# Performance work log

Hardware: AMD Instinct MI355X
Metric: run time of the kernel (lower is better)

The kernel has to match this reference:

```python
import jax, jax.numpy as jnp
import numpy as np

B, C, H, W = 64, 64, 64, 64
KD = 64  # kernel_dim == res == dim (required by the torch reshapes)


def _ln(t, g, b, eps=1e-5):
    mu = jnp.mean(t, axis=-1, keepdims=True)
    var = jnp.var(t, axis=-1, keepdims=True)
    return (t - mu) * jax.lax.rsqrt(var + eps) * g + b


def _cos_map(n, kd):
    i = jnp.arange(n, dtype=jnp.float32)[:, None]
    j = jnp.arange(kd, dtype=jnp.float32)[None, :]
    return jnp.cos(i * j * jnp.pi / n) / kd


def setup_inputs() -> dict:
    key = jax.random.key(0)
    ks = jax.random.split(key, 6)
    s = 0.02
    return {
        "x": jax.random.normal(ks[0], (B, C, H, W), jnp.float32),
        "freq_embed": jax.random.normal(ks[1], (H, W, C), jnp.float32),
        "g_k": jnp.ones((C,), jnp.float32), "b_k": jnp.zeros((C,), jnp.float32),
        "Wk": jax.random.normal(ks[2], (C, KD), jnp.float32) * s, "bk": jnp.zeros((KD,), jnp.float32),
        "g_z": jnp.ones((C,), jnp.float32), "b_z": jnp.zeros((C,), jnp.float32),
        "Wz": jax.random.normal(ks[3], (C, C), jnp.float32) * s, "bz": jnp.zeros((C,), jnp.float32),
        "g_o": jnp.ones((KD,), jnp.float32), "b_o": jnp.zeros((KD,), jnp.float32),
        "Wo": jax.random.normal(ks[4], (KD, C), jnp.float32) * s, "bo": jnp.zeros((C,), jnp.float32),
    }


def reference(x, freq_embed, g_k, b_k, Wk, bk, g_z, b_z, Wz, bz, g_o, b_o, Wo, bo):
    # x: (B,C,H,W) -> (B,H,W,C), matching the torch permute branch
    x = jnp.transpose(x, (0, 2, 3, 1))
    Bc, Hc, Wc, Cc = x.shape
    kd = Wk.shape[1]
    xin = x + freq_embed[None]                    # freq_embed broadcast over batch
    k = _ln(xin, g_k, b_k) @ Wk + bk              # (B,H,W,kd)
    z = _ln(freq_embed, g_z, b_z) @ Wz + bz       # to_k(freq_embed): (H,W,C)
    cosn = _cos_map(Hc, kd)                       # (H,kd)
    cosm = _cos_map(Wc, kd)                       # (W,kd)
    i = jnp.arange(Hc, dtype=jnp.float32)[:, None]
    j = jnp.arange(Wc, dtype=jnp.float32)[None, :]
    decay = (jnp.exp(-(i + j) / max(Hc, Wc)) / kd).astype(x.dtype)  # (H,W)
    wexp = decay[:, :, None] ** z                 # (H,W,C), decay > 0
    # separable forward DCT (two kernel-1 conv1d == two contractions)
    t = jnp.einsum('nh,bhwc->bnwc', cosn, k)
    t = jnp.einsum('mw,bnwc->bnmc', cosm, t)
    t = t * wexp[None]                            # exponential-decay spectral gate
    # separable inverse DCT
    t = jnp.einsum('nh,bnmc->bhmc', cosn, t)
    t = jnp.einsum('mw,bhmc->bhwc', cosm, t)
    out = _ln(t, g_o, b_o) * jax.nn.silu(z)[None]
    out = out @ Wo + bo
    return jnp.transpose(out, (0, 3, 1, 2))       # back to BCHW
```

## Files before the change

kernel.cpp:

```cpp
#include <hip/hip_runtime.h>


#define PADR 68

typedef __attribute__((ext_vector_type(8))) short short8;
typedef __attribute__((ext_vector_type(4))) float f32x4;
typedef __attribute__((ext_vector_type(4))) unsigned short us4;

__device__ __forceinline__ unsigned short bfhi(float f) {
    return (unsigned short)(__builtin_bit_cast(unsigned int, f) >> 16);
}
__device__ __forceinline__ float hif(float f) {
    return __builtin_bit_cast(float, __builtin_bit_cast(unsigned int, f) & 0xFFFF0000u);
}
__device__ __forceinline__ int swa(int row, int col) {
    return (row << 7) + (((col >> 3) ^ (row & 7)) << 4) + ((col & 7) << 1);
}
__device__ __forceinline__ short8 fragrd(const short* buf, int row, int kc) {
    int a = (row << 7) + (((kc ^ (row & 7)) << 4));
    return *(const short8*)((const char*)buf + a);
}

__device__ __forceinline__ void fma16(float (&acc)[4][4], float4 a, float4 b) {
    acc[0][0] = fmaf(a.x, b.x, acc[0][0]);
    acc[0][1] = fmaf(a.x, b.y, acc[0][1]);
    acc[0][2] = fmaf(a.x, b.z, acc[0][2]);
    acc[0][3] = fmaf(a.x, b.w, acc[0][3]);
    acc[1][0] = fmaf(a.y, b.x, acc[1][0]);
    acc[1][1] = fmaf(a.y, b.y, acc[1][1]);
    acc[1][2] = fmaf(a.y, b.z, acc[1][2]);
    acc[1][3] = fmaf(a.y, b.w, acc[1][3]);
    acc[2][0] = fmaf(a.z, b.x, acc[2][0]);
    acc[2][1] = fmaf(a.z, b.y, acc[2][1]);
    acc[2][2] = fmaf(a.z, b.z, acc[2][2]);
    acc[2][3] = fmaf(a.z, b.w, acc[2][3]);
    acc[3][0] = fmaf(a.w, b.x, acc[3][0]);
    acc[3][1] = fmaf(a.w, b.y, acc[3][1]);
    acc[3][2] = fmaf(a.w, b.z, acc[3][2]);
    acc[3][3] = fmaf(a.w, b.w, acc[3][3]);
}

__global__ void k_cos(unsigned short* __restrict__ chi, unsigned short* __restrict__ clo) {
    int i = blockIdx.x, j = threadIdx.x;
    float ang = (float)(i * j) * 3.14159265358979323846f * (1.0f / 64.0f);
    float v = cosf(ang) * (1.0f / 64.0f);
    chi[i * 64 + j] = bfhi(v);
    clo[i * 64 + j] = bfhi(v - hif(v));
}

__global__ void k_z(const float* __restrict__ freq, const float* __restrict__ g_z,
                    const float* __restrict__ b_z, const float* __restrict__ Wz,
                    const float* __restrict__ bz,
                    float* __restrict__ siluzT, float* __restrict__ wexpT) {
    int hw = blockIdx.x;
    int h = hw >> 6, w = hw & 63;
    int c = threadIdx.x;
    float f = freq[hw * 64 + c];
    float s = f;
    #pragma unroll
    for (int off = 32; off > 0; off >>= 1) s += __shfl_xor(s, off, 64);
    float mu = s * (1.0f / 64.0f);
    float d = f - mu;
    float s2 = d * d;
    #pragma unroll
    for (int off = 32; off > 0; off >>= 1) s2 += __shfl_xor(s2, off, 64);
    float var = s2 * (1.0f / 64.0f);
    float xn = d * rsqrtf(var + 1e-5f) * g_z[c] + b_z[c];
    __shared__ float xnS[64];
    xnS[c] = xn;
    __syncthreads();
    float acc = bz[c];
    #pragma unroll 8
    for (int c2 = 0; c2 < 64; ++c2) acc = fmaf(xnS[c2], Wz[c2 * 64 + c], acc);
    float zc = acc;
    siluzT[c * 4096 + hw] = zc / (1.0f + expf(-zc));
    float lnd = -(float)(h + w) * (1.0f / 64.0f) - 4.1588830833596718565f;
    wexpT[c * 4096 + hw] = expf(zc * lnd);
}

__global__ __launch_bounds__(256) void k_k(
    const float* __restrict__ x, const float* __restrict__ freq,
    const float* __restrict__ g_k, const float* __restrict__ b_k,
    const float* __restrict__ Wk, const float* __restrict__ bk,
    float* __restrict__ planes) {
    int b = blockIdx.x >> 6, h = blockIdx.x & 63;
    __shared__ __align__(16) float xsT[64][PADR];
    __shared__ __align__(16) float WkS[64][PADR];
    __shared__ __align__(16) float red1[4][PADR], red2[4][PADR];
    __shared__ __align__(16) float muS[64], rsS[64];
    int t = threadIdx.x;

    #pragma unroll
    for (int i = 0; i < 4; ++i) {
        int e = t + i * 256;
        int row = e >> 4, col = (e & 15) << 2;
        *(float4*)&WkS[row][col] = *(const float4*)&Wk[row * 64 + col];
    }
    const float* xb = x + (b * 64 * 64 + h) * 64;
    const float* fh = freq + h * 4096;
    #pragma unroll
    for (int i = 0; i < 4; ++i) {
        int e = t + i * 256;
        int c = e >> 4, w = (e & 15) << 2;
        float4 xv = *(const float4*)&xb[c * 4096 + w];
        xv.x += fh[(w + 0) * 64 + c];
        xv.y += fh[(w + 1) * 64 + c];
        xv.z += fh[(w + 2) * 64 + c];
        xv.w += fh[(w + 3) * 64 + c];
        *(float4*)&xsT[c][w] = xv;
    }
    __syncthreads();
    {
        int w = t & 63, q = t >> 6;
        float s1 = 0.f, s2 = 0.f;
        #pragma unroll
        for (int k = 0; k < 16; ++k) { float v = xsT[q * 16 + k][w]; s1 += v; s2 += v * v; }
        red1[q][w] = s1; red2[q][w] = s2;
    }
    __syncthreads();
    if (t < 64) {
        float s1 = red1[0][t] + red1[1][t] + red1[2][t] + red1[3][t];
        float s2 = red2[0][t] + red2[1][t] + red2[2][t] + red2[3][t];
        float mu = s1 * (1.0f / 64.0f);
        float var = s2 * (1.0f / 64.0f) - mu * mu;
        muS[t] = mu; rsS[t] = rsqrtf(var + 1e-5f);
    }
    __syncthreads();
    #pragma unroll
    for (int i = 0; i < 4; ++i) {
        int e = t + i * 256;
        int c = e >> 4, w = (e & 15) << 2;
        float gk = g_k[c], bkc = b_k[c];
        float4 v = *(float4*)&xsT[c][w];
        float4 mu = *(const float4*)&muS[w];
        float4 rs = *(const float4*)&rsS[w];
        v.x = (v.x - mu.x) * rs.x * gk + bkc;
        v.y = (v.y - mu.y) * rs.y * gk + bkc;
        v.z = (v.z - mu.z) * rs.z * gk + bkc;
        v.w = (v.w - mu.w) * rs.w * gk + bkc;
        *(float4*)&xsT[c][w] = v;
    }
    __syncthreads();
    int p = t & 15, g = t >> 4;
    int w0 = p << 2, n0 = g << 2;
    float4 bkv = *(const float4*)&bk[n0];
    float acc[4][4];
    #pragma unroll
    for (int i = 0; i < 4; ++i) { acc[i][0] = bkv.x; acc[i][1] = bkv.y; acc[i][2] = bkv.z; acc[i][3] = bkv.w; }
    #pragma unroll 8
    for (int c = 0; c < 64; ++c) {
        float4 a = *(const float4*)&xsT[c][w0];
        float4 bb = *(const float4*)&WkS[c][n0];
        fma16(acc, a, bb);
    }
    #pragma unroll
    for (int j = 0; j < 4; ++j) {
        float4 v = make_float4(acc[0][j], acc[1][j], acc[2][j], acc[3][j]);
        *(float4*)&planes[((b * 64 + n0 + j) * 64 + h) * 64 + w0] = v;
    }
}

__global__ __launch_bounds__(256, 3) void k_spec(
    float* __restrict__ planes,
    const unsigned short* __restrict__ cos_hi, const unsigned short* __restrict__ cos_lo,
    const float* __restrict__ wexpT) {
    __shared__ short Ch[4096], Cl[4096];
    __shared__ short D0h[4096], D0l[4096];
    __shared__ short D1h[4096], D1l[4096];
    int b = blockIdx.x >> 6, c = blockIdx.x & 63;
    float* po = planes + (b * 64 + c) * 4096;
    int t = threadIdx.x;
    int lane = t & 63, wv = t >> 6;
    int q = lane >> 4, l15 = lane & 15;
    int m0 = (wv & 1) << 5, n0 = (wv >> 1) << 5;

    {
        int r = t >> 2, cb = (t & 3) << 4;
        #pragma unroll
        for (int p = 0; p < 2; ++p) {
            int chunk = (cb >> 3) + p;
            int a = (r << 7) + (((chunk ^ (r & 7)) << 4));
            *(uint4*)((char*)Ch + a) = *(const uint4*)&cos_hi[r * 64 + cb + p * 8];
            *(uint4*)((char*)Cl + a) = *(const uint4*)&cos_lo[r * 64 + cb + p * 8];
        }
    }
    {
        int w = t & 63, h0 = (t >> 6) << 4;
        float v[16];
        #pragma unroll
        for (int j = 0; j < 16; ++j) v[j] = po[(h0 + j) * 64 + w];
        #pragma unroll
        for (int g = 0; g < 4; ++g) {
            int col = h0 + (g << 2);
            int a = swa(w, col);
            us4 hv, lv;
            #pragma unroll
            for (int r = 0; r < 4; ++r) {
                float f = v[(g << 2) + r];
                hv[r] = bfhi(f);
                lv[r] = bfhi(f - hif(f));
            }
            *(us4*)((char*)D0h + a) = hv;
            *(us4*)((char*)D0l + a) = lv;
        }
    }
    __syncthreads();

    f32x4 acc[2][2];
    const f32x4 zero = {0.f, 0.f, 0.f, 0.f};

#define MM(Ah, Al, Bh, Bl)                                                          \
    {                                                                               \
        acc[0][0] = zero; acc[0][1] = zero; acc[1][0] = zero; acc[1][1] = zero;     \
        _Pragma("unroll")                                                           \
        for (int kb = 0; kb < 2; ++kb) {                                            \
            int kc = (kb << 2) + q;                                                 \
            short8 a0h = fragrd(Ah, m0 + l15, kc);                                  \
            short8 a0l = fragrd(Al, m0 + l15, kc);                                  \
            short8 a1h = fragrd(Ah, m0 + 16 + l15, kc);                             \
            short8 a1l = fragrd(Al, m0 + 16 + l15, kc);                             \
            short8 b0h = fragrd(Bh, n0 + l15, kc);                                  \
            short8 b0l = fragrd(Bl, n0 + l15, kc);                                  \
            short8 b1h = fragrd(Bh, n0 + 16 + l15, kc);                             \
            short8 b1l = fragrd(Bl, n0 + 16 + l15, kc);                             \
            acc[0][0] = __builtin_amdgcn_mfma_f32_16x16x32_bf16(a0h, b0h, acc[0][0], 0, 0, 0); \
            acc[0][0] = __builtin_amdgcn_mfma_f32_16x16x32_bf16(a0h, b0l, acc[0][0], 0, 0, 0); \
            acc[0][0] = __builtin_amdgcn_mfma_f32_16x16x32_bf16(a0l, b0h, acc[0][0], 0, 0, 0); \
            acc[0][1] = __builtin_amdgcn_mfma_f32_16x16x32_bf16(a0h, b1h, acc[0][1], 0, 0, 0); \
            acc[0][1] = __builtin_amdgcn_mfma_f32_16x16x32_bf16(a0h, b1l, acc[0][1], 0, 0, 0); \
            acc[0][1] = __builtin_amdgcn_mfma_f32_16x16x32_bf16(a0l, b1h, acc[0][1], 0, 0, 0); \
            acc[1][0] = __builtin_amdgcn_mfma_f32_16x16x32_bf16(a1h, b0h, acc[1][0], 0, 0, 0); \
            acc[1][0] = __builtin_amdgcn_mfma_f32_16x16x32_bf16(a1h, b0l, acc[1][0], 0, 0, 0); \
            acc[1][0] = __builtin_amdgcn_mfma_f32_16x16x32_bf16(a1l, b0h, acc[1][0], 0, 0, 0); \
            acc[1][1] = __builtin_amdgcn_mfma_f32_16x16x32_bf16(a1h, b1h, acc[1][1], 0, 0, 0); \
            acc[1][1] = __builtin_amdgcn_mfma_f32_16x16x32_bf16(a1h, b1l, acc[1][1], 0, 0, 0); \
            acc[1][1] = __builtin_amdgcn_mfma_f32_16x16x32_bf16(a1l, b1h, acc[1][1], 0, 0, 0); \
        }                                                                           \
    }

#define WB_T(Dh, Dl)                                                                \
    {                                                                               \
        _Pragma("unroll")                                                           \
        for (int ti = 0; ti < 2; ++ti)                                              \
            _Pragma("unroll")                                                       \
            for (int u = 0; u < 2; ++u) {                                           \
                int row = n0 + (u << 4) + l15;                                      \
                int col = m0 + (ti << 4) + (q << 2);                                \
                int a = swa(row, col);                                              \
                us4 hv, lv;                                                         \
                _Pragma("unroll")                                                   \
                for (int r = 0; r < 4; ++r) {                                       \
                    float f = acc[ti][u][r];                                        \
                    hv[r] = bfhi(f);                                                \
                    lv[r] = bfhi(f - hif(f));                                       \
                }                                                                   \
                *(us4*)((char*)Dh + a) = hv;                                        \
                *(us4*)((char*)Dl + a) = lv;                                        \
            }                                                                       \
    }

    MM(D0h, D0l, Ch, Cl)
    WB_T(D1h, D1l)
    __syncthreads();

    MM(D1h, D1l, Ch, Cl)
    {
        const float* wx = wexpT + c * 4096;
        #pragma unroll
        for (int ti = 0; ti < 2; ++ti)
            #pragma unroll
            for (int u = 0; u < 2; ++u)
                #pragma unroll
                for (int r = 0; r < 4; ++r) {
                    int n = m0 + (ti << 4) + (q << 2) + r;
                    int m = n0 + (u << 4) + l15;
                    acc[ti][u][r] *= wx[n * 64 + m];
                }
    }
    WB_T(D0h, D0l)
    __syncthreads();

    MM(Ch, Cl, D0h, D0l)
    {
        #pragma unroll
        for (int ti = 0; ti < 2; ++ti)
            #pragma unroll
            for (int u = 0; u < 2; ++u)
                #pragma unroll
                for (int r = 0; r < 4; ++r) {
                    int row = m0 + (ti << 4) + (q << 2) + r;
                    int col = n0 + (u << 4) + l15;
                    int a = swa(row, col);
                    float f = acc[ti][u][r];
                    *(unsigned short*)((char*)D1h + a) = bfhi(f);
                    *(unsigned short*)((char*)D1l + a) = bfhi(f - hif(f));
                }
    }
    __syncthreads();

    MM(D1h, D1l, Ch, Cl)
    {
        #pragma unroll
        for (int ti = 0; ti < 2; ++ti)
            #pragma unroll
            for (int u = 0; u < 2; ++u)
                #pragma unroll
                for (int r = 0; r < 4; ++r) {
                    int h = m0 + (ti << 4) + (q << 2) + r;
                    int w = n0 + (u << 4) + l15;
                    po[h * 64 + w] = acc[ti][u][r];
                }
    }
#undef MM
#undef WB_T
}

__global__ __launch_bounds__(256) void k_out(
    const float* __restrict__ planes, const float* __restrict__ siluzT,
    const float* __restrict__ g_o, const float* __restrict__ b_o,
    const float* __restrict__ Wo, const float* __restrict__ bo,
    float* __restrict__ out) {
    int b = blockIdx.x >> 6, h = blockIdx.x & 63;
    __shared__ __align__(16) float tsT[64][PADR];
    __shared__ __align__(16) float WoS[64][PADR];
    __shared__ __align__(16) float red1[4][PADR], red2[4][PADR];
    __shared__ __align__(16) float muS[64], rsS[64];
    int t = threadIdx.x;

    #pragma unroll
    for (int i = 0; i < 4; ++i) {
        int e = t + i * 256;
        int row = e >> 4, col = (e & 15) << 2;
        *(float4*)&WoS[row][col] = *(const float4*)&Wo[row * 64 + col];
    }
    const float* pb = planes + (b * 64 * 64) * 64 + h * 64;
    #pragma unroll
    for (int i = 0; i < 4; ++i) {
        int e = t + i * 256;
        int c = e >> 4, w = (e & 15) << 2;
        *(float4*)&tsT[c][w] = *(const float4*)&pb[c * 4096 + w];
    }
    __syncthreads();
    {
        int w = t & 63, q = t >> 6;
        float s1 = 0.f, s2 = 0.f;
        #pragma unroll
        for (int k = 0; k < 16; ++k) { float v = tsT[q * 16 + k][w]; s1 += v; s2 += v * v; }
        red1[q][w] = s1; red2[q][w] = s2;
    }
    __syncthreads();
    if (t < 64) {
        float s1 = red1[0][t] + red1[1][t] + red1[2][t] + red1[3][t];
        float s2 = red2[0][t] + red2[1][t] + red2[2][t] + red2[3][t];
        float mu = s1 * (1.0f / 64.0f);
        float var = s2 * (1.0f / 64.0f) - mu * mu;
        muS[t] = mu; rsS[t] = rsqrtf(var + 1e-5f);
    }
    __syncthreads();
    const float* sz = siluzT + h * 64;
    #pragma unroll
    for (int i = 0; i < 4; ++i) {
        int e = t + i * 256;
        int c = e >> 4, w = (e & 15) << 2;
        float go = g_o[c], boc = b_o[c];
        float4 v = *(float4*)&tsT[c][w];
        float4 mu = *(const float4*)&muS[w];
        float4 rs = *(const float4*)&rsS[w];
        float4 sv = *(const float4*)&sz[c * 4096 + w];
        v.x = ((v.x - mu.x) * rs.x * go + boc) * sv.x;
        v.y = ((v.y - mu.y) * rs.y * go + boc) * sv.y;
        v.z = ((v.z - mu.z) * rs.z * go + boc) * sv.z;
        v.w = ((v.w - mu.w) * rs.w * go + boc) * sv.w;
        *(float4*)&tsT[c][w] = v;
    }
    __syncthreads();
    int p = t & 15, g = t >> 4;
    int w0 = p << 2, o0 = g << 2;
    float4 bov = *(const float4*)&bo[o0];
    float acc[4][4];
    #pragma unroll
    for (int i = 0; i < 4; ++i) { acc[i][0] = bov.x; acc[i][1] = bov.y; acc[i][2] = bov.z; acc[i][3] = bov.w; }
    #pragma unroll 8
    for (int c = 0; c < 64; ++c) {
        float4 a = *(const float4*)&tsT[c][w0];
        float4 bb = *(const float4*)&WoS[c][o0];
        fma16(acc, a, bb);
    }
    #pragma unroll
    for (int j = 0; j < 4; ++j) {
        float4 v = make_float4(acc[0][j], acc[1][j], acc[2][j], acc[3][j]);
        *(float4*)&out[((b * 64 + o0 + j) * 64 + h) * 64 + w0] = v;
    }
}

extern "C" void kernel_launch(void* const* d_in, const int* in_sizes, int n_in,
                              void* d_out, int out_size, void* d_ws, size_t ws_size,
                              hipStream_t stream) {
    const float* x    = (const float*)d_in[0];
    const float* freq = (const float*)d_in[1];
    const float* g_k  = (const float*)d_in[2];
    const float* b_k  = (const float*)d_in[3];
    const float* Wk   = (const float*)d_in[4];
    const float* bk   = (const float*)d_in[5];
    const float* g_z  = (const float*)d_in[6];
    const float* b_z  = (const float*)d_in[7];
    const float* Wz   = (const float*)d_in[8];
    const float* bz   = (const float*)d_in[9];
    const float* g_o  = (const float*)d_in[10];
    const float* b_o  = (const float*)d_in[11];
    const float* Wo   = (const float*)d_in[12];
    const float* bo   = (const float*)d_in[13];
    float* out = (float*)d_out;

    float* ws = (float*)d_ws;
    float* planes = ws;
    float* siluzT = planes + 16777216;
    float* wexpT  = siluzT + 262144;
    unsigned short* cos_hi = (unsigned short*)(wexpT + 262144);
    unsigned short* cos_lo = cos_hi + 4096;

    k_cos<<<64, 64, 0, stream>>>(cos_hi, cos_lo);
    k_z<<<4096, 64, 0, stream>>>(freq, g_z, b_z, Wz, bz, siluzT, wexpT);
    k_k<<<4096, 256, 0, stream>>>(x, freq, g_k, b_k, Wk, bk, planes);
    k_spec<<<4096, 256, 0, stream>>>(planes, cos_hi, cos_lo, wexpT);
    k_out<<<4096, 256, 0, stream>>>(planes, siluzT, g_o, b_o, Wo, bo, out);
}
```

Measured before the change: 241.6 us.

## Move channel projections to split-bf16 MFMA with LayerNorm folded into weights

The three 64x64 channel projections (to_k on x, to_k on freq_embed, and the output projection) now run on bf16x3 MFMA tiles instead of scalar FP32 FMA loops. The LayerNorm gain and bias are folded into precomputed transposed weights plus per-column sum and bias vectors, so the normalisation becomes a cheap epilogue. freq_embed is pre-transposed once so the k kernel can read it coalesced. The setup kernels are merged, and k_k and k_out drop a shared-memory pass and gain a 3-blocks-per-CU launch bound. The bf16 hi/lo split keeps accuracy close to FP32, but folding LayerNorm into the epilogue can lose some precision.

```diff
diff --git a/kernel.cpp b/kernel.cpp
--- a/kernel.cpp
+++ b/kernel.cpp
@@ -1,7 +1,5 @@
 #include <hip/hip_runtime.h>
 
-
-#define PADR 68
 
 typedef __attribute__((ext_vector_type(8))) short short8;
 typedef __attribute__((ext_vector_type(4))) float f32x4;
@@ -17,146 +15,266 @@
     return (row << 7) + (((col >> 3) ^ (row & 7)) << 4) + ((col & 7) << 1);
 }
 __device__ __forceinline__ short8 fragrd(const short* buf, int row, int kc) {
-    int a = (row << 7) + (((kc ^ (row & 7)) << 4));
+    int a = (row << 7) + ((kc ^ (row & 7)) << 4);
     return *(const short8*)((const char*)buf + a);
 }
 
-__device__ __forceinline__ void fma16(float (&acc)[4][4], float4 a, float4 b) {
-    acc[0][0] = fmaf(a.x, b.x, acc[0][0]);
-    acc[0][1] = fmaf(a.x, b.y, acc[0][1]);
-    acc[0][2] = fmaf(a.x, b.z, acc[0][2]);
-    acc[0][3] = fmaf(a.x, b.w, acc[0][3]);
-    acc[1][0] = fmaf(a.y, b.x, acc[1][0]);
-    acc[1][1] = fmaf(a.y, b.y, acc[1][1]);
-    acc[1][2] = fmaf(a.y, b.z, acc[1][2]);
-    acc[1][3] = fmaf(a.y, b.w, acc[1][3]);
-    acc[2][0] = fmaf(a.z, b.x, acc[2][0]);
-    acc[2][1] = fmaf(a.z, b.y, acc[2][1]);
-    acc[2][2] = fmaf(a.z, b.z, acc[2][2]);
-    acc[2][3] = fmaf(a.z, b.w, acc[2][3]);
-    acc[3][0] = fmaf(a.w, b.x, acc[3][0]);
-    acc[3][1] = fmaf(a.w, b.y, acc[3][1]);
-    acc[3][2] = fmaf(a.w, b.z, acc[3][2]);
-    acc[3][3] = fmaf(a.w, b.w, acc[3][3]);
-}
-
-__global__ void k_cos(unsigned short* __restrict__ chi, unsigned short* __restrict__ clo) {
-    int i = blockIdx.x, j = threadIdx.x;
-    float ang = (float)(i * j) * 3.14159265358979323846f * (1.0f / 64.0f);
-    float v = cosf(ang) * (1.0f / 64.0f);
-    chi[i * 64 + j] = bfhi(v);
-    clo[i * 64 + j] = bfhi(v - hif(v));
-}
-
-__global__ void k_z(const float* __restrict__ freq, const float* __restrict__ g_z,
-                    const float* __restrict__ b_z, const float* __restrict__ Wz,
-                    const float* __restrict__ bz,
-                    float* __restrict__ siluzT, float* __restrict__ wexpT) {
-    int hw = blockIdx.x;
-    int h = hw >> 6, w = hw & 63;
-    int c = threadIdx.x;
-    float f = freq[hw * 64 + c];
-    float s = f;
-    #pragma unroll
-    for (int off = 32; off > 0; off >>= 1) s += __shfl_xor(s, off, 64);
-    float mu = s * (1.0f / 64.0f);
-    float d = f - mu;
-    float s2 = d * d;
-    #pragma unroll
-    for (int off = 32; off > 0; off >>= 1) s2 += __shfl_xor(s2, off, 64);
-    float var = s2 * (1.0f / 64.0f);
-    float xn = d * rsqrtf(var + 1e-5f) * g_z[c] + b_z[c];
-    __shared__ float xnS[64];
-    xnS[c] = xn;
-    __syncthreads();
-    float acc = bz[c];
-    #pragma unroll 8
-    for (int c2 = 0; c2 < 64; ++c2) acc = fmaf(xnS[c2], Wz[c2 * 64 + c], acc);
-    float zc = acc;
-    siluzT[c * 4096 + hw] = zc / (1.0f + expf(-zc));
-    float lnd = -(float)(h + w) * (1.0f / 64.0f) - 4.1588830833596718565f;
-    wexpT[c * 4096 + hw] = expf(zc * lnd);
-}
-
-__global__ __launch_bounds__(256) void k_k(
-    const float* __restrict__ x, const float* __restrict__ freq,
+__device__ __forceinline__ void mm_block(const short* Ah, const short* Al,
+                                         const short* Bh, const short* Bl,
+                                         int m0, int n0, int l15, int q,
+                                         f32x4 (&acc)[2][2]) {
+    const f32x4 zero = {0.f, 0.f, 0.f, 0.f};
+    acc[0][0] = zero; acc[0][1] = zero; acc[1][0] = zero; acc[1][1] = zero;
+    #pragma unroll
+    for (int kb = 0; kb < 2; ++kb) {
+        int kc = (kb << 2) + q;
+        short8 a0h = fragrd(Ah, m0 + l15, kc);
+        short8 a0l = fragrd(Al, m0 + l15, kc);
+        short8 a1h = fragrd(Ah, m0 + 16 + l15, kc);
+        short8 a1l = fragrd(Al, m0 + 16 + l15, kc);
+        short8 b0h = fragrd(Bh, n0 + l15, kc);
+        short8 b0l = fragrd(Bl, n0 + l15, kc);
+        short8 b1h = fragrd(Bh, n0 + 16 + l15, kc);
+        short8 b1l = fragrd(Bl, n0 + 16 + l15, kc);
+        acc[0][0] = __builtin_amdgcn_mfma_f32_16x16x32_bf16(a0h, b0h, acc[0][0], 0, 0, 0);
+        acc[0][0] = __builtin_amdgcn_mfma_f32_16x16x32_bf16(a0h, b0l, acc[0][0], 0, 0, 0);
+        acc[0][0] = __builtin_amdgcn_mfma_f32_16x16x32_bf16(a0l, b0h, acc[0][0], 0, 0, 0);
+        acc[0][1] = __builtin_amdgcn_mfma_f32_16x16x32_bf16(a0h, b1h, acc[0][1], 0, 0, 0);
+        acc[0][1] = __builtin_amdgcn_mfma_f32_16x16x32_bf16(a0h, b1l, acc[0][1], 0, 0, 0);
+        acc[0][1] = __builtin_amdgcn_mfma_f32_16x16x32_bf16(a0l, b1h, acc[0][1], 0, 0, 0);
+        acc[1][0] = __builtin_amdgcn_mfma_f32_16x16x32_bf16(a1h, b0h, acc[1][0], 0, 0, 0);
+        acc[1][0] = __builtin_amdgcn_mfma_f32_16x16x32_bf16(a1h, b0l, acc[1][0], 0, 0, 0);
+        acc[1][0] = __builtin_amdgcn_mfma_f32_16x16x32_bf16(a1l, b0h, acc[1][0], 0, 0, 0);
+        acc[1][1] = __builtin_amdgcn_mfma_f32_16x16x32_bf16(a1h, b1h, acc[1][1], 0, 0, 0);
+        acc[1][1] = __builtin_amdgcn_mfma_f32_16x16x32_bf16(a1h, b1l, acc[1][1], 0, 0, 0);
+        acc[1][1] = __builtin_amdgcn_mfma_f32_16x16x32_bf16(a1l, b1h, acc[1][1], 0, 0, 0);
+    }
+}
+
+__global__ __launch_bounds__(256) void k_pre1(
     const float* __restrict__ g_k, const float* __restrict__ b_k,
     const float* __restrict__ Wk, const float* __restrict__ bk,
-    float* __restrict__ planes) {
-    int b = blockIdx.x >> 6, h = blockIdx.x & 63;
-    __shared__ __align__(16) float xsT[64][PADR];
-    __shared__ __align__(16) float WkS[64][PADR];
-    __shared__ __align__(16) float red1[4][PADR], red2[4][PADR];
-    __shared__ __align__(16) float muS[64], rsS[64];
+    const float* __restrict__ g_z, const float* __restrict__ b_z,
+    const float* __restrict__ Wz, const float* __restrict__ bz,
+    const float* __restrict__ Wo,
+    unsigned short* __restrict__ WkTh, unsigned short* __restrict__ WkTl,
+    float* __restrict__ su_k, float* __restrict__ v_k,
+    unsigned short* __restrict__ WzTh, unsigned short* __restrict__ WzTl,
+    float* __restrict__ su_z, float* __restrict__ v_z,
+    unsigned short* __restrict__ WoTh, unsigned short* __restrict__ WoTl,
+    unsigned short* __restrict__ cos_hi, unsigned short* __restrict__ cos_lo) {
     int t = threadIdx.x;
-
-    #pragma unroll
-    for (int i = 0; i < 4; ++i) {
-        int e = t + i * 256;
-        int row = e >> 4, col = (e & 15) << 2;
-        *(float4*)&WkS[row][col] = *(const float4*)&Wk[row * 64 + col];
-    }
-    const float* xb = x + (b * 64 * 64 + h) * 64;
-    const float* fh = freq + h * 4096;
-    #pragma unroll
-    for (int i = 0; i < 4; ++i) {
-        int e = t + i * 256;
-        int c = e >> 4, w = (e & 15) << 2;
-        float4 xv = *(const float4*)&xb[c * 4096 + w];
-        xv.x += fh[(w + 0) * 64 + c];
-        xv.y += fh[(w + 1) * 64 + c];
-        xv.z += fh[(w + 2) * 64 + c];
-        xv.w += fh[(w + 3) * 64 + c];
-        *(float4*)&xsT[c][w] = xv;
-    }
-    __syncthreads();
-    {
-        int w = t & 63, q = t >> 6;
+    if (blockIdx.x < 16) {
+        int n = blockIdx.x * 4 + (t >> 6);
+        int c = t & 63;
+        float wk = Wk[c * 64 + n];
+        float a = g_k[c] * wk;
+        WkTh[n * 64 + c] = bfhi(a);
+        WkTl[n * 64 + c] = bfhi(a - hif(a));
+        float sa = a, sv = b_k[c] * wk;
+        #pragma unroll
+        for (int off = 32; off > 0; off >>= 1) {
+            sa += __shfl_xor(sa, off, 64);
+            sv += __shfl_xor(sv, off, 64);
+        }
+        if (c == 0) { su_k[n] = sa; v_k[n] = sv + bk[n]; }
+        float wz = Wz[c * 64 + n];
+        float az = g_z[c] * wz;
+        WzTh[n * 64 + c] = bfhi(az);
+        WzTl[n * 64 + c] = bfhi(az - hif(az));
+        float saz = az, svz = b_z[c] * wz;
+        #pragma unroll
+        for (int off = 32; off > 0; off >>= 1) {
+            saz += __shfl_xor(saz, off, 64);
+            svz += __shfl_xor(svz, off, 64);
+        }
+        if (c == 0) { su_z[n] = saz; v_z[n] = svz + bz[n]; }
+        float wo = Wo[c * 64 + n];
+        WoTh[n * 64 + c] = bfhi(wo);
+        WoTl[n * 64 + c] = bfhi(wo - hif(wo));
+    } else {
+        int idx = (blockIdx.x - 16) * 256 + t;
+        int i = idx >> 6, j = idx & 63;
+        float ang = (float)(i * j) * 3.14159265358979323846f * (1.0f / 64.0f);
+        float v = cosf(ang) * (1.0f / 64.0f);
+        cos_hi[idx] = bfhi(v);
+        cos_lo[idx] = bfhi(v - hif(v));
+    }
+}
+
+__global__ __launch_bounds__(256) void k_pre2(
+    const float* __restrict__ freq,
+    const unsigned short* __restrict__ WzTh_g, const unsigned short* __restrict__ WzTl_g,
+    const float* __restrict__ su_z, const float* __restrict__ v_z,
+    float* __restrict__ siluzT, float* __restrict__ wexpT,
+    float* __restrict__ freqT) {
+    __shared__ short Ah[4096], Al[4096], Bh[4096], Bl[4096];
+    __shared__ float muS[64], rsS[64];
+    __shared__ float tile[64][65];
+    int t = threadIdx.x;
+    if (blockIdx.x < 64) {
+        int h = blockIdx.x;
+        #pragma unroll
+        for (int p = 0; p < 2; ++p) {
+            int e = t + p * 256;
+            int row = e >> 3, ch = e & 7;
+            int a = (row << 7) + (((ch ^ (row & 7)) << 4));
+            *(uint4*)((char*)Bh + a) = *(const uint4*)&WzTh_g[row * 64 + ch * 8];
+            *(uint4*)((char*)Bl + a) = *(const uint4*)&WzTl_g[row * 64 + ch * 8];
+        }
+        int w = t >> 2, c0 = (t & 3) << 4;
+        float4 fr[4];
         float s1 = 0.f, s2 = 0.f;
         #pragma unroll
-        for (int k = 0; k < 16; ++k) { float v = xsT[q * 16 + k][w]; s1 += v; s2 += v * v; }
-        red1[q][w] = s1; red2[q][w] = s2;
-    }
-    __syncthreads();
-    if (t < 64) {
-        float s1 = red1[0][t] + red1[1][t] + red1[2][t] + red1[3][t];
-        float s2 = red2[0][t] + red2[1][t] + red2[2][t] + red2[3][t];
+        for (int i = 0; i < 4; ++i) {
+            fr[i] = *(const float4*)&freq[(h * 64 + w) * 64 + c0 + 4 * i];
+            s1 += fr[i].x + fr[i].y + fr[i].z + fr[i].w;
+            s2 += fr[i].x * fr[i].x + fr[i].y * fr[i].y + fr[i].z * fr[i].z + fr[i].w * fr[i].w;
+        }
+        s1 += __shfl_xor(s1, 1, 64); s1 += __shfl_xor(s1, 2, 64);
+        s2 += __shfl_xor(s2, 1, 64); s2 += __shfl_xor(s2, 2, 64);
         float mu = s1 * (1.0f / 64.0f);
         float var = s2 * (1.0f / 64.0f) - mu * mu;
+        float rs = rsqrtf(var + 1e-5f);
+        if ((t & 3) == 0) { muS[w] = mu; rsS[w] = rs; }
+        const float* fp = (const float*)fr;
+        #pragma unroll
+        for (int i = 0; i < 4; ++i) {
+            us4 hv, lv;
+            #pragma unroll
+            for (int r = 0; r < 4; ++r) {
+                float f = fp[i * 4 + r];
+                hv[r] = bfhi(f);
+                lv[r] = bfhi(f - hif(f));
+            }
+            int a = swa(w, c0 + 4 * i);
+            *(us4*)((char*)Ah + a) = hv;
+            *(us4*)((char*)Al + a) = lv;
+        }
+        __syncthreads();
+        int lane = t & 63, wv = t >> 6;
+        int q = lane >> 4, l15 = lane & 15;
+        int m0 = (wv & 1) << 5, n0 = (wv >> 1) << 5;
+        f32x4 acc[2][2];
+        mm_block(Ah, Al, Bh, Bl, m0, n0, l15, q, acc);
+        #pragma unroll
+        for (int u = 0; u < 2; ++u) {
+            int c = n0 + (u << 4) + l15;
+            float suc = su_z[c], vc = v_z[c];
+            #pragma unroll
+            for (int ti = 0; ti < 2; ++ti) {
+                int wb = m0 + (ti << 4) + (q << 2);
+                float4 mu4 = *(const float4*)&muS[wb];
+                float4 rs4 = *(const float4*)&rsS[wb];
+                float4 sil, wx;
+                #pragma unroll
+                for (int r = 0; r < 4; ++r) {
+                    float z = ((const float*)&rs4)[r] * (acc[ti][u][r] - ((const float*)&mu4)[r] * suc) + vc;
+                    float lnd = -(float)(h + wb + r) * 0.015625f - 4.1588830833596718565f;
+                    ((float*)&sil)[r] = z / (1.0f + expf(-z));
+                    ((float*)&wx)[r] = expf(z * lnd);
+                }
+                int base = (c * 64 + h) * 64 + wb;
+                *(float4*)&siluzT[base] = sil;
+                *(float4*)&wexpT[base] = wx;
+            }
+        }
+    } else {
+        int h = blockIdx.x - 64;
+        int w = t >> 2, c0 = (t & 3) << 4;
+        #pragma unroll
+        for (int i = 0; i < 4; ++i)
+            *(float4*)&tile[w][c0 + 4 * i] = *(const float4*)&freq[(h * 64 + w) * 64 + c0 + 4 * i];
+        __syncthreads();
+        int w0 = (t & 15) << 2;
+        #pragma unroll
+        for (int p = 0; p < 4; ++p) {
+            int c = (t >> 4) + 16 * p;
+            float4 fv = make_float4(tile[w0][c], tile[w0 + 1][c], tile[w0 + 2][c], tile[w0 + 3][c]);
+            *(float4*)&freqT[(c * 64 + h) * 64 + w0] = fv;
+        }
+    }
+}
+
+__global__ __launch_bounds__(256, 3) void k_k(
+    const float* __restrict__ x, const float* __restrict__ freqT,
+    const unsigned short* __restrict__ WkTh_g, const unsigned short* __restrict__ WkTl_g,
+    const float* __restrict__ su_k, const float* __restrict__ v_k,
+    float* __restrict__ planes) {
+    __shared__ short Ah[4096], Al[4096], Bh[4096], Bl[4096];
+    __shared__ __align__(16) float red1[16][68], red2[16][68];
+    __shared__ float muS[64], rsS[64];
+    int b = blockIdx.x >> 6, h = blockIdx.x & 63;
+    int t = threadIdx.x;
+    #pragma unroll
+    for (int p = 0; p < 2; ++p) {
+        int e = t + p * 256;
+        int row = e >> 3, ch = e & 7;
+        int a = (row << 7) + (((ch ^ (row & 7)) << 4));
+        *(uint4*)((char*)Bh + a) = *(const uint4*)&WkTh_g[row * 64 + ch * 8];
+        *(uint4*)((char*)Bl + a) = *(const uint4*)&WkTl_g[row * 64 + ch * 8];
+    }
+    int g = t >> 4, w0 = (t & 15) << 2, c0 = g << 2;
+    const float* xb = x + (size_t)b * 262144 + h * 64;
+    float4 vr[4];
+    float4 s1 = {0,0,0,0}, s2 = {0,0,0,0};
+    #pragma unroll
+    for (int i = 0; i < 4; ++i) {
+        int c = c0 + i;
+        float4 xv = *(const float4*)&xb[c * 4096 + w0];
+        float4 fv = *(const float4*)&freqT[c * 4096 + h * 64 + w0];
+        xv.x += fv.x; xv.y += fv.y; xv.z += fv.z; xv.w += fv.w;
+        vr[i] = xv;
+        s1.x += xv.x; s1.y += xv.y; s1.z += xv.z; s1.w += xv.w;
+        s2.x += xv.x * xv.x; s2.y += xv.y * xv.y; s2.z += xv.z * xv.z; s2.w += xv.w * xv.w;
+    }
+    const float* vp = (const float*)vr;
+    #pragma unroll
+    for (int j = 0; j < 4; ++j) {
+        us4 hv, lv;
+        #pragma unroll
+        for (int r = 0; r < 4; ++r) {
+            float f = vp[r * 4 + j];
+            hv[r] = bfhi(f);
+            lv[r] = bfhi(f - hif(f));
+        }
+        int a = swa(w0 + j, c0);
+        *(us4*)((char*)Ah + a) = hv;
+        *(us4*)((char*)Al + a) = lv;
+    }
+    *(float4*)&red1[g][w0] = s1;
+    *(float4*)&red2[g][w0] = s2;
+    __syncthreads();
+    if (t < 64) {
+        float a1 = 0.f, a2 = 0.f;
+        #pragma unroll
+        for (int j = 0; j < 16; ++j) { a1 += red1[j][t]; a2 += red2[j][t]; }
+        float mu = a1 * (1.0f / 64.0f);
+        float var = a2 * (1.0f / 64.0f) - mu * mu;
         muS[t] = mu; rsS[t] = rsqrtf(var + 1e-5f);
     }
     __syncthreads();
-    #pragma unroll
-    for (int i = 0; i < 4; ++i) {
-        int e = t + i * 256;
-        int c = e >> 4, w = (e & 15) << 2;
-        float gk = g_k[c], bkc = b_k[c];
-        float4 v = *(float4*)&xsT[c][w];
-        float4 mu = *(const float4*)&muS[w];
-        float4 rs = *(const float4*)&rsS[w];
-        v.x = (v.x - mu.x) * rs.x * gk + bkc;
-        v.y = (v.y - mu.y) * rs.y * gk + bkc;
-        v.z = (v.z - mu.z) * rs.z * gk + bkc;
-        v.w = (v.w - mu.w) * rs.w * gk + bkc;
-        *(float4*)&xsT[c][w] = v;
-    }
-    __syncthreads();
-    int p = t & 15, g = t >> 4;
-    int w0 = p << 2, n0 = g << 2;
-    float4 bkv = *(const float4*)&bk[n0];
-    float acc[4][4];
-    #pragma unroll
-    for (int i = 0; i < 4; ++i) { acc[i][0] = bkv.x; acc[i][1] = bkv.y; acc[i][2] = bkv.z; acc[i][3] = bkv.w; }
-    #pragma unroll 8
-    for (int c = 0; c < 64; ++c) {
-        float4 a = *(const float4*)&xsT[c][w0];
-        float4 bb = *(const float4*)&WkS[c][n0];
-        fma16(acc, a, bb);
-    }
-    #pragma unroll
-    for (int j = 0; j < 4; ++j) {
-        float4 v = make_float4(acc[0][j], acc[1][j], acc[2][j], acc[3][j]);
-        *(float4*)&planes[((b * 64 + n0 + j) * 64 + h) * 64 + w0] = v;
+    int lane = t & 63, wv = t >> 6;
+    int q = lane >> 4, l15 = lane & 15;
+    int m0 = (wv & 1) << 5, n0 = (wv >> 1) << 5;
+    f32x4 acc[2][2];
+    mm_block(Ah, Al, Bh, Bl, m0, n0, l15, q, acc);
+    #pragma unroll
+    for (int u = 0; u < 2; ++u) {
+        int n = n0 + (u << 4) + l15;
+        float sun = su_k[n], vn = v_k[n];
+        #pragma unroll
+        for (int ti = 0; ti < 2; ++ti) {
+            int wb = m0 + (ti << 4) + (q << 2);
+            float4 mu4 = *(const float4*)&muS[wb];
+            float4 rs4 = *(const float4*)&rsS[wb];
+            float4 o;
+            o.x = rs4.x * (acc[ti][u][0] - mu4.x * sun) + vn;
+            o.y = rs4.y * (acc[ti][u][1] - mu4.y * sun) + vn;
+            o.z = rs4.z * (acc[ti][u][2] - mu4.z * sun) + vn;
+            o.w = rs4.w * (acc[ti][u][3] - mu4.w * sun) + vn;
+            *(float4*)&planes[((size_t)(b * 64 + n) * 64 + h) * 64 + wb] = o;
+        }
     }
 }
 
@@ -168,7 +286,7 @@
     __shared__ short D0h[4096], D0l[4096];
     __shared__ short D1h[4096], D1l[4096];
     int b = blockIdx.x >> 6, c = blockIdx.x & 63;
-    float* po = planes + (b * 64 + c) * 4096;
+    float* po = planes + (size_t)(b * 64 + c) * 4096;
     int t = threadIdx.x;
     int lane = t & 63, wv = t >> 6;
     int q = lane >> 4, l15 = lane & 15;
@@ -207,36 +325,6 @@
     __syncthreads();
 
     f32x4 acc[2][2];
-    const f32x4 zero = {0.f, 0.f, 0.f, 0.f};
-
-#define MM(Ah, Al, Bh, Bl)                                                          \
-    {                                                                               \
-        acc[0][0] = zero; acc[0][1] = zero; acc[1][0] = zero; acc[1][1] = zero;     \
-        _Pragma("unroll")                                                           \
-        for (int kb = 0; kb < 2; ++kb) {                                            \
-            int kc = (kb << 2) + q;                                                 \
-            short8 a0h = fragrd(Ah, m0 + l15, kc);                                  \
-            short8 a0l = fragrd(Al, m0 + l15, kc);                                  \
-            short8 a1h = fragrd(Ah, m0 + 16 + l15, kc);                             \
-            short8 a1l = fragrd(Al, m0 + 16 + l15, kc);                             \
-            short8 b0h = fragrd(Bh, n0 + l15, kc);                                  \
-            short8 b0l = fragrd(Bl, n0 + l15, kc);                                  \
-            short8 b1h = fragrd(Bh, n0 + 16 + l15, kc);                             \
-            short8 b1l = fragrd(Bl, n0 + 16 + l15, kc);                             \
-            acc[0][0] = __builtin_amdgcn_mfma_f32_16x16x32_bf16(a0h, b0h, acc[0][0], 0, 0, 0); \
-            acc[0][0] = __builtin_amdgcn_mfma_f32_16x16x32_bf16(a0h, b0l, acc[0][0], 0, 0, 0); \
-            acc[0][0] = __builtin_amdgcn_mfma_f32_16x16x32_bf16(a0l, b0h, acc[0][0], 0, 0, 0); \
-            acc[0][1] = __builtin_amdgcn_mfma_f32_16x16x32_bf16(a0h, b1h, acc[0][1], 0, 0, 0); \
-            acc[0][1] = __builtin_amdgcn_mfma_f32_16x16x32_bf16(a0h, b1l, acc[0][1], 0, 0, 0); \
-            acc[0][1] = __builtin_amdgcn_mfma_f32_16x16x32_bf16(a0l, b1h, acc[0][1], 0, 0, 0); \
-            acc[1][0] = __builtin_amdgcn_mfma_f32_16x16x32_bf16(a1h, b0h, acc[1][0], 0, 0, 0); \
-            acc[1][0] = __builtin_amdgcn_mfma_f32_16x16x32_bf16(a1h, b0l, acc[1][0], 0, 0, 0); \
-            acc[1][0] = __builtin_amdgcn_mfma_f32_16x16x32_bf16(a1l, b0h, acc[1][0], 0, 0, 0); \
-            acc[1][1] = __builtin_amdgcn_mfma_f32_16x16x32_bf16(a1h, b1h, acc[1][1], 0, 0, 0); \
-            acc[1][1] = __builtin_amdgcn_mfma_f32_16x16x32_bf16(a1h, b1l, acc[1][1], 0, 0, 0); \
-            acc[1][1] = __builtin_amdgcn_mfma_f32_16x16x32_bf16(a1l, b1h, acc[1][1], 0, 0, 0); \
-        }                                                                           \
-    }
 
 #define WB_T(Dh, Dl)                                                                \
     {                                                                               \
@@ -259,13 +347,12 @@
             }                                                                       \
     }
 
-    MM(D0h, D0l, Ch, Cl)
+    mm_block(D0h, D0l, Ch, Cl, m0, n0, l15, q, acc);
     WB_T(D1h, D1l)
     __syncthreads();
-
-    MM(D1h, D1l, Ch, Cl)
+    mm_block(D1h, D1l, Ch, Cl, m0, n0, l15, q, acc);
     {
-        const float* wx = wexpT + c * 4096;
+        const float* wx = wexpT + (size_t)c * 4096;
         #pragma unroll
         for (int ti = 0; ti < 2; ++ti)
             #pragma unroll
@@ -279,8 +366,7 @@
     }
     WB_T(D0h, D0l)
     __syncthreads();
-
-    MM(Ch, Cl, D0h, D0l)
+    mm_block(Ch, Cl, D0h, D0l, m0, n0, l15, q, acc);
     {
         #pragma unroll
         for (int ti = 0; ti < 2; ++ti)
@@ -297,8 +383,7 @@
                 }
     }
     __syncthreads();
-
-    MM(D1h, D1l, Ch, Cl)
+    mm_block(D1h, D1l, Ch, Cl, m0, n0, l15, q, acc);
     {
         #pragma unroll
         for (int ti = 0; ti < 2; ++ti)
@@ -311,85 +396,99 @@
                     po[h * 64 + w] = acc[ti][u][r];
                 }
     }
-#undef MM
 #undef WB_T
 }
 
-__global__ __launch_bounds__(256) void k_out(
+__global__ __launch_bounds__(256, 3) void k_out(
     const float* __restrict__ planes, const float* __restrict__ siluzT,
     const float* __restrict__ g_o, const float* __restrict__ b_o,
-    const float* __restrict__ Wo, const float* __restrict__ bo,
-    float* __restrict__ out) {
+    const unsigned short* __restrict__ WoTh_g, const unsigned short* __restrict__ WoTl_g,
+    const float* __restrict__ bo, float* __restrict__ out) {
+    __shared__ short Ah[4096], Al[4096], Bh[4096], Bl[4096];
+    __shared__ __align__(16) float red1[16][68], red2[16][68];
+    __shared__ float muS[64], rsS[64];
     int b = blockIdx.x >> 6, h = blockIdx.x & 63;
-    __shared__ __align__(16) float tsT[64][PADR];
-    __shared__ __align__(16) float WoS[64][PADR];
-    __shared__ __align__(16) float red1[4][PADR], red2[4][PADR];
-    __shared__ __align__(16) float muS[64], rsS[64];
     int t = threadIdx.x;
-
+    #pragma unroll
+    for (int p = 0; p < 2; ++p) {
+        int e = t + p * 256;
+        int row = e >> 3, ch = e & 7;
+        int a = (row << 7) + (((ch ^ (row & 7)) << 4));
+        *(uint4*)((char*)Bh + a) = *(const uint4*)&WoTh_g[row * 64 + ch * 8];
+        *(uint4*)((char*)Bl + a) = *(const uint4*)&WoTl_g[row * 64 + ch * 8];
+    }
+    int g = t >> 4, w0 = (t & 15) << 2, c0 = g << 2;
+    const float* pb = planes + (size_t)b * 262144 + h * 64;
+    float4 vr[4], szr[4];
+    float4 s1 = {0,0,0,0}, s2 = {0,0,0,0};
     #pragma unroll
     for (int i = 0; i < 4; ++i) {
-        int e = t + i * 256;
-        int row = e >> 4, col = (e & 15) << 2;
-        *(float4*)&WoS[row][col] = *(const float4*)&Wo[row * 64 + col];
-    }
-    const float* pb = planes + (b * 64 * 64) * 64 + h * 64;
-    #pragma unroll
-    for (int i = 0; i < 4; ++i) {
-        int e = t + i * 256;
-        int c = e >> 4, w = (e & 15) << 2;
-        *(float4*)&tsT[c][w] = *(const float4*)&pb[c * 4096 + w];
+        int c = c0 + i;
+        float4 tv = *(const float4*)&pb[c * 4096 + w0];
+        szr[i] = *(const float4*)&siluzT[c * 4096 + h * 64 + w0];
+        vr[i] = tv;
+        s1.x += tv.x; s1.y += tv.y; s1.z += tv.z; s1.w += tv.w;
+        s2.x += tv.x * tv.x; s2.y += tv.y * tv.y; s2.z += tv.z * tv.z; s2.w += tv.w * tv.w;
+    }
+    *(float4*)&red1[g][w0] = s1;
+    *(float4*)&red2[g][w0] = s2;
+    __syncthreads();
+    if (t < 64) {
+        float a1 = 0.f, a2 = 0.f;
+        #pragma unroll
+        for (int j = 0; j < 16; ++j) { a1 += red1[j][t]; a2 += red2[j][t]; }
+        float mu = a1 * (1.0f / 64.0f);
+        float var = a2 * (1.0f / 64.0f) - mu * mu;
+        muS[t] = mu; rsS[t] = rsqrtf(var + 1e-5f);
     }
     __syncthreads();
     {
-        int w = t & 63, q = t >> 6;
-        float s1 = 0.f, s2 = 0.f;
-        #pragma unroll
-        for (int k = 0; k < 16; ++k) { float v = tsT[q * 16 + k][w]; s1 += v; s2 += v * v; }
-        red1[q][w] = s1; red2[q][w] = s2;
-    }
-    __syncthreads();
-    if (t < 64) {
-        float s1 = red1[0][t] + red1[1][t] + red1[2][t] + red1[3][t];
-        float s2 = red2[0][t] + red2[1][t] + red2[2][t] + red2[3][t];
-        float mu = s1 * (1.0f / 64.0f);
-        float var = s2 * (1.0f / 64.0f) - mu * mu;
-        muS[t] = mu; rsS[t] = rsqrtf(var + 1e-5f);
-    }
-    __syncthreads();
-    const float* sz = siluzT + h * 64;
-    #pragma unroll
-    for (int i = 0; i < 4; ++i) {
-        int e = t + i * 256;
-        int c = e >> 4, w = (e & 15) << 2;
-        float go = g_o[c], boc = b_o[c];
-        float4 v = *(float4*)&tsT[c][w];
-        float4 mu = *(const float4*)&muS[w];
-        float4 rs = *(const float4*)&rsS[w];
-        float4 sv = *(const float4*)&sz[c * 4096 + w];
-        v.x = ((v.x - mu.x) * rs.x * go + boc) * sv.x;
-        v.y = ((v.y - mu.y) * rs.y * go + boc) * sv.y;
-        v.z = ((v.z - mu.z) * rs.z * go + boc) * sv.z;
-        v.w = ((v.w - mu.w) * rs.w * go + boc) * sv.w;
-        *(float4*)&tsT[c][w] = v;
-    }
-    __syncthreads();
-    int p = t & 15, g = t >> 4;
-    int w0 = p << 2, o0 = g << 2;
-    float4 bov = *(const float4*)&bo[o0];
-    float acc[4][4];
-    #pragma unroll
-    for (int i = 0; i < 4; ++i) { acc[i][0] = bov.x; acc[i][1] = bov.y; acc[i][2] = bov.z; acc[i][3] = bov.w; }
-    #pragma unroll 8
-    for (int c = 0; c < 64; ++c) {
-        float4 a = *(const float4*)&tsT[c][w0];
-        float4 bb = *(const float4*)&WoS[c][o0];
-        fma16(acc, a, bb);
-    }
-    #pragma unroll
-    for (int j = 0; j < 4; ++j) {
-        float4 v = make_float4(acc[0][j], acc[1][j], acc[2][j], acc[3][j]);
-        *(float4*)&out[((b * 64 + o0 + j) * 64 + h) * 64 + w0] = v;
+        float4 mu4 = *(const float4*)&muS[w0];
+        float4 rs4 = *(const float4*)&rsS[w0];
+        #pragma unroll
+        for (int i = 0; i < 4; ++i) {
+            int c = c0 + i;
+            float go = g_o[c], boc = b_o[c];
+            vr[i].x = ((vr[i].x - mu4.x) * rs4.x * go + boc) * szr[i].x;
+            vr[i].y = ((vr[i].y - mu4.y) * rs4.y * go + boc) * szr[i].y;
+            vr[i].z = ((vr[i].z - mu4.z) * rs4.z * go + boc) * szr[i].z;
+            vr[i].w = ((vr[i].w - mu4.w) * rs4.w * go + boc) * szr[i].w;
+        }
+        const float* vp = (const float*)vr;
+        #pragma unroll
+        for (int j = 0; j < 4; ++j) {
+            us4 hv, lv;
+            #pragma unroll
+            for (int r = 0; r < 4; ++r) {
+                float f = vp[r * 4 + j];
+                hv[r] = bfhi(f);
+                lv[r] = bfhi(f - hif(f));
+            }
+            int a = swa(w0 + j, c0);
+            *(us4*)((char*)Ah + a) = hv;
+            *(us4*)((char*)Al + a) = lv;
+        }
+    }
+    __syncthreads();
+    int lane = t & 63, wv = t >> 6;
+    int q = lane >> 4, l15 = lane & 15;
+    int m0 = (wv & 1) << 5, n0 = (wv >> 1) << 5;
+    f32x4 acc[2][2];
+    mm_block(Ah, Al, Bh, Bl, m0, n0, l15, q, acc);
+    #pragma unroll
+    for (int u = 0; u < 2; ++u) {
+        int o_ = n0 + (u << 4) + l15;
+        float bov = bo[o_];
+        #pragma unroll
+        for (int ti = 0; ti < 2; ++ti) {
+            int wb = m0 + (ti << 4) + (q << 2);
+            float4 o;
+            o.x = acc[ti][u][0] + bov;
+            o.y = acc[ti][u][1] + bov;
+            o.z = acc[ti][u][2] + bov;
+            o.w = acc[ti][u][3] + bov;
+            *(float4*)&out[((size_t)(b * 64 + o_) * 64 + h) * 64 + wb] = o;
+        }
     }
 }
 
@@ -416,12 +515,25 @@
     float* planes = ws;
     float* siluzT = planes + 16777216;
     float* wexpT  = siluzT + 262144;
-    unsigned short* cos_hi = (unsigned short*)(wexpT + 262144);
+    float* freqT  = wexpT + 262144;
+    float* su_k   = freqT + 262144;
+    float* v_k    = su_k + 64;
+    float* su_z   = v_k + 64;
+    float* v_z    = su_z + 64;
+    unsigned short* cos_hi = (unsigned short*)(v_z + 64);
     unsigned short* cos_lo = cos_hi + 4096;
-
-    k_cos<<<64, 64, 0, stream>>>(cos_hi, cos_lo);
-    k_z<<<4096, 64, 0, stream>>>(freq, g_z, b_z, Wz, bz, siluzT, wexpT);
-    k_k<<<4096, 256, 0, stream>>>(x, freq, g_k, b_k, Wk, bk, planes);
+    unsigned short* WkTh = cos_lo + 4096;
+    unsigned short* WkTl = WkTh + 4096;
+    unsigned short* WzTh = WkTl + 4096;
+    unsigned short* WzTl = WzTh + 4096;
+    unsigned short* WoTh = WzTl + 4096;
+    unsigned short* WoTl = WoTh + 4096;
+
+    k_pre1<<<32, 256, 0, stream>>>(g_k, b_k, Wk, bk, g_z, b_z, Wz, bz, Wo,
+                                   WkTh, WkTl, su_k, v_k, WzTh, WzTl, su_z, v_z,
+                                   WoTh, WoTl, cos_hi, cos_lo);
+    k_pre2<<<128, 256, 0, stream>>>(freq, WzTh, WzTl, su_z, v_z, siluzT, wexpT, freqT);
+    k_k<<<4096, 256, 0, stream>>>(x, freqT, WkTh, WkTl, su_k, v_k, planes);
     k_spec<<<4096, 256, 0, stream>>>(planes, cos_hi, cos_lo, wexpT);
-    k_out<<<4096, 256, 0, stream>>>(planes, siluzT, g_o, b_o, Wo, bo, out);
-}
+    k_out<<<4096, 256, 0, stream>>>(planes, siluzT, g_o, b_o, WoTh, WoTl, bo, out);
+}
```

New measurement: 210.7 us. -12.8%, faster.
